# Kernel optimization log

Hardware: AMD Instinct MI355X
Metric: run time of the kernel (lower is better)

Reference implementation:

```python
import jax, jax.numpy as jnp
import numpy as np

N_HEADS = 16
EPS = 1e-5

def _ln(h, g, b):
    mu = jnp.mean(h, axis=-1, keepdims=True)
    var = jnp.var(h, axis=-1, keepdims=True)
    return (h - mu) * jax.lax.rsqrt(var + EPS) * g + b

def setup_inputs() -> dict:
    key = jax.random.key(0)
    ks = jax.random.split(key, 8)
    B, S, D, M = 2, 2048, 2048, 8192
    x = jax.random.normal(ks[0], (B, S, D), dtype=jnp.float32)
    # causal mask: True where attention is disallowed (j > i)
    mask = jnp.triu(jnp.ones((S, S), dtype=bool), k=1)[None, None]
    s = 1.0 / np.sqrt(D)
    Wq = jax.random.normal(ks[1], (D, D), dtype=jnp.float32) * s
    Wk = jax.random.normal(ks[2], (D, D), dtype=jnp.float32) * s
    Wv = jax.random.normal(ks[3], (D, D), dtype=jnp.float32) * s
    Wo = jax.random.normal(ks[4], (D, D), dtype=jnp.float32) * s
    W1 = jax.random.normal(ks[5], (D, M), dtype=jnp.float32) * s
    b1 = jnp.zeros((M,), dtype=jnp.float32)
    W2 = jax.random.normal(ks[6], (M, D), dtype=jnp.float32) * (1.0 / np.sqrt(M))
    b2 = jnp.zeros((D,), dtype=jnp.float32)
    ln1_g = jnp.ones((D,), jnp.float32); ln1_b = jnp.zeros((D,), jnp.float32)
    ln2_g = jnp.ones((D,), jnp.float32); ln2_b = jnp.zeros((D,), jnp.float32)
    return dict(x=x, self_attn_mask=mask, Wq=Wq, Wk=Wk, Wv=Wv, Wo=Wo,
                ln1_g=ln1_g, ln1_b=ln1_b, W1=W1, b1=b1, W2=W2, b2=b2,
                ln2_g=ln2_g, ln2_b=ln2_b)

def reference(x, self_attn_mask, Wq, Wk, Wv, Wo, ln1_g, ln1_b, W1, b1, W2, b2, ln2_g, ln2_b):
    B, S, D = x.shape
    n = N_HEADS
    d = D // n
    # --- self-attention with pre-norm residual ---
    h = _ln(x, ln1_g, ln1_b)
    # NOTE: source uses .view(b, n_heads, i, head_dim) with NO transpose -> plain reshape
    q = (h @ Wq).reshape(B, n, S, d)
    k = (h @ Wk).reshape(B, n, S, d)
    v = (h @ Wv).reshape(B, n, S, d)
    score = jnp.einsum('bnid,bnjd->bnij', q, k)
    # NOTE: source masks BEFORE scaling, so -1e9 is also divided by sqrt(d)
    score = jnp.where(self_attn_mask, jnp.float32(-1e9), score) / jnp.sqrt(jnp.float32(d))
    w = jax.nn.softmax(score, axis=3)
    o = jnp.einsum('bnij,bnjd->bnid', w, v)
    o = o.transpose(0, 2, 1, 3).reshape(B, S, D)  # b n i d -> b i (n d)
    x = x + o @ Wo
    # --- FFN with pre-norm residual ---
    h2 = _ln(x, ln2_g, ln2_b)
    ff = jnp.maximum(h2 @ W1 + b1, 0.0) @ W2 + b2
    return x + ff
```

## Files before the change

### kernel.cpp

```cpp
#include <hip/hip_runtime.h>
#include <cstdint>

using bf16x8 = __attribute__((ext_vector_type(8))) short;
using f32x4  = __attribute__((ext_vector_type(4))) float;

__device__ __forceinline__ unsigned short f2bf(float f) {
  union { float f; unsigned u; } v; v.f = f;
  unsigned u = v.u;
  u += 0x7fffu + ((u >> 16) & 1u);
  return (unsigned short)(u >> 16);
}

__device__ __forceinline__ void gload_lds16(const unsigned short* g, unsigned short* l) {
  __builtin_amdgcn_global_load_lds(
      (const __attribute__((address_space(1))) unsigned int*)g,
      (__attribute__((address_space(3))) unsigned int*)l, 16, 0, 0);
}

__global__ __launch_bounds__(256) void ln_kernel(
    const float* __restrict__ x, const float* __restrict__ g,
    const float* __restrict__ bb, unsigned short* __restrict__ h)
{
  const int D = 2048;
  const int row = blockIdx.x;
  const float* xr = x + (size_t)row * D;
  const int t = threadIdx.x;
  float4 v0 = ((const float4*)xr)[t];
  float4 v1 = ((const float4*)xr)[t + 256];
  float s  = v0.x+v0.y+v0.z+v0.w + v1.x+v1.y+v1.z+v1.w;
  float ss = v0.x*v0.x+v0.y*v0.y+v0.z*v0.z+v0.w*v0.w
           + v1.x*v1.x+v1.y*v1.y+v1.z*v1.z+v1.w*v1.w;
  #pragma unroll
  for (int off = 1; off < 64; off <<= 1) {
    s  += __shfl_xor(s, off);
    ss += __shfl_xor(ss, off);
  }
  __shared__ float red[8];
  const int wave = t >> 6, lane = t & 63;
  if (lane == 0) { red[wave] = s; red[4+wave] = ss; }
  __syncthreads();
  s  = red[0]+red[1]+red[2]+red[3];
  ss = red[4]+red[5]+red[6]+red[7];
  const float mu   = s * (1.f/2048.f);
  const float var  = ss * (1.f/2048.f) - mu*mu;
  const float rstd = rsqrtf(var + 1e-5f);
  unsigned short* hr = h + (size_t)row * D;
  #pragma unroll
  for (int q = 0; q < 2; ++q) {
    float4 v = q ? v1 : v0;
    int vecidx = t + q*256;
    float4 gg  = ((const float4*)g)[vecidx];
    float4 bv  = ((const float4*)bb)[vecidx];
    ushort4 o;
    o.x = f2bf((v.x-mu)*rstd*gg.x + bv.x);
    o.y = f2bf((v.y-mu)*rstd*gg.y + bv.y);
    o.z = f2bf((v.z-mu)*rstd*gg.z + bv.z);
    o.w = f2bf((v.w-mu)*rstd*gg.w + bv.w);
    *(ushort4*)(hr + vecidx*4) = o;
  }
}

__global__ __launch_bounds__(256) void transpose_cast(
    const float* __restrict__ W, unsigned short* __restrict__ WT,
    int K, int N)
{
  __shared__ float tile[32][33];
  const int tx = threadIdx.x, ty = threadIdx.y;
  const int n0 = blockIdx.x * 32, k0 = blockIdx.y * 32;
  #pragma unroll
  for (int r = 0; r < 4; ++r)
    tile[ty + r*8][tx] = W[(size_t)(k0 + ty + r*8) * N + n0 + tx];
  __syncthreads();
  #pragma unroll
  for (int r = 0; r < 4; ++r)
    WT[(size_t)(n0 + ty + r*8) * K + k0 + tx] = f2bf(tile[tx][ty + r*8]);
}

template<int BN, bool BIAS, bool RELU, bool RESID, bool OUTBF16>
__global__ __launch_bounds__(512, 2) void gemm8(
    const unsigned short* __restrict__ A, const unsigned short* __restrict__ BT,
    const float* __restrict__ bias, const float* __restrict__ resid,
    void* __restrict__ Cp, int M, int N, int K, int nbx)
{
  constexpr int BM = 256, BK = 64;
  constexpr int NREP = BN / 64;
  constexpr int BLD  = BN / 64;
  constexpr int LPK  = 4 + BLD;
  __shared__ __align__(16) unsigned short lds[2][(BM + BN) * BK];

  const int tid  = threadIdx.x;
  const int lane = tid & 63, wave = tid >> 6;
  const int l15 = lane & 15, lh = lane >> 4;
  const int wr = wave >> 2, wc = wave & 3;

  const int nwg = gridDim.x;
  const int q8  = nwg >> 3;
  const int wg  = blockIdx.x;
  const int swz = (wg & 7) * q8 + (wg >> 3);
  const size_t bm = (size_t)(swz / nbx) * BM;
  const size_t bn = (size_t)(swz % nbx) * BN;

  const int nk = K >> 6;

  auto stage = [&](int buf, int kt) {
    unsigned short* La = &lds[buf][0];
    unsigned short* Lb = &lds[buf][BM * BK];
    #pragma unroll
    for (int qq = 0; qq < 4; ++qq) {
      int idx = qq * 512 + tid;
      int row = idx >> 3, c = idx & 7;
      int gc = c ^ (row & 7);
      gload_lds16(A + (bm + row) * (size_t)K + (size_t)kt * BK + gc * 8,
                  La + idx * 8);
    }
    #pragma unroll
    for (int qq = 0; qq < BLD; ++qq) {
      int idx = qq * 512 + tid;
      int row = idx >> 3, c = idx & 7;
      int gc = c ^ (row & 7);
      gload_lds16(BT + (bn + row) * (size_t)K + (size_t)kt * BK + gc * 8,
                  Lb + idx * 8);
    }
  };

  f32x4 acc[8][NREP] = {};

  stage(0, 0);
  stage(1, 1);

  for (int kt = 0; kt < nk; ++kt) {
    const int buf = kt & 1;
    if (kt < nk - 1) {
      asm volatile("s_waitcnt vmcnt(%0)" :: "i"(LPK) : "memory");
    } else {
      asm volatile("s_waitcnt vmcnt(0)" ::: "memory");
    }
    __builtin_amdgcn_s_barrier();
    asm volatile("" ::: "memory");

    const unsigned short* La = &lds[buf][0];
    const unsigned short* Lb = &lds[buf][BM * BK];
    bf16x8 bfr[2][NREP];
    #pragma unroll
    for (int p = 0; p < 4; ++p) {
      if (p == 0) {
        #pragma unroll
        for (int kk = 0; kk < 2; ++kk)
          #pragma unroll
          for (int n = 0; n < NREP; ++n) {
            int brow = wc * (BN / 4) + n * 16 + l15;
            bfr[kk][n] = *(const bf16x8*)(Lb + brow * 64 +
                           ((kk * 32 + lh * 8) ^ ((brow & 7) << 3)));
          }
      }
      bf16x8 af[2][2];
      #pragma unroll
      for (int mi = 0; mi < 2; ++mi) {
        int arow = wr * 128 + (p * 2 + mi) * 16 + l15;
        #pragma unroll
        for (int kk = 0; kk < 2; ++kk)
          af[mi][kk] = *(const bf16x8*)(La + arow * 64 +
                         ((kk * 32 + lh * 8) ^ ((arow & 7) << 3)));
      }
      asm volatile("" ::: "memory");
      __builtin_amdgcn_s_barrier();
      __builtin_amdgcn_s_setprio(1);
      #pragma unroll
      for (int mi = 0; mi < 2; ++mi)
        #pragma unroll
        for (int n = 0; n < NREP; ++n)
          #pragma unroll
          for (int kk = 0; kk < 2; ++kk)
            acc[p*2+mi][n] = __builtin_amdgcn_mfma_f32_16x16x32_bf16(
                af[mi][kk], bfr[kk][n], acc[p*2+mi][n], 0, 0, 0);
      __builtin_amdgcn_s_setprio(0);
      asm volatile("" ::: "memory");
      __builtin_amdgcn_s_barrier();
    }
    if (kt + 2 < nk) stage(buf, kt + 2);
  }

  float bv[NREP];
  if (BIAS) {
    #pragma unroll
    for (int n = 0; n < NREP; ++n) bv[n] = bias[bn + wc*(BN/4) + n*16 + l15];
  }
  #pragma unroll
  for (int m = 0; m < 8; ++m) {
    #pragma unroll
    for (int r = 0; r < 4; ++r) {
      size_t rrow = bm + wr*128 + m*16 + lh*4 + r;
      #pragma unroll
      for (int n = 0; n < NREP; ++n) {
        size_t ccol = bn + wc*(BN/4) + n*16 + l15;
        float v = acc[m][n][r];
        if (BIAS)  v += bv[n];
        if (RELU)  v = fmaxf(v, 0.f);
        if (RESID) v += resid[rrow*(size_t)N + ccol];
        if (OUTBF16) ((unsigned short*)Cp)[rrow*(size_t)N + ccol] = f2bf(v);
        else         ((float*)Cp)[rrow*(size_t)N + ccol] = v;
      }
    }
  }
}

__global__ __launch_bounds__(256) void attn_kernel(
    const unsigned short* __restrict__ QKV, unsigned short* __restrict__ O)
{
  constexpr float SCALE = 0.08838834764831845f;
  __shared__ __align__(16) unsigned short Kl[64*128];
  __shared__ __align__(16) unsigned short Vf[64*128];
  __shared__ __align__(16) unsigned short Pl[4*1024];
  const int bid = blockIdx.x;
  const int qt = 31 - (bid >> 5);
  const int nh = bid & 15;
  const int b  = (bid >> 4) & 1;
  const int t = threadIdx.x;
  const int lane = t & 63, wave = t >> 6;
  const int l15 = lane & 15, lh = lane >> 4;
  const int i0 = qt*64 + wave*16;
  const size_t RS = 6144;
  const size_t base = (size_t)b * 2048 * RS;

  const unsigned short* qrow = QKV + base + (size_t)(nh*128 + (i0 >> 4)) * RS;
  bf16x8 qf[4];
  #pragma unroll
  for (int c = 0; c < 4; ++c)
    qf[c] = *(const bf16x8*)(qrow + l15*128 + c*32 + lh*8);

  f32x4 of[8] = {};
  float mrun[4], lrun[4];
  #pragma unroll
  for (int r = 0; r < 4; ++r) { mrun[r] = -INFINITY; lrun[r] = 0.f; }

  const int nkt = qt + 1;
  bf16x8 kr[4], vr[4];
  auto loadKV = [&](int kt) {
    #pragma unroll
    for (int q = 0; q < 4; ++q) {
      int c = t + q*256;
      int j = c >> 4, dd0 = (c & 15) * 8;
      const size_t grow = base + (size_t)(nh*128 + kt*4 + (j >> 4)) * RS + (j & 15)*128 + dd0;
      kr[q] = *(const bf16x8*)(QKV + grow + 2048);
      vr[q] = *(const bf16x8*)(QKV + grow + 4096);
    }
  };
  loadKV(0);

  for (int kt = 0; kt < nkt; ++kt) {
    __syncthreads();
    #pragma unroll
    for (int q = 0; q < 4; ++q) {
      int c = t + q*256;
      int j = c >> 4, dd0 = (c & 15) * 8;
      *(bf16x8*)((char*)Kl + ((j*256 + dd0*2) ^ ((j & 7) << 4))) = kr[q];
      int ks = j >> 5, jq = j & 31;
      int cc = dd0 >> 4;
      int wb = ks*8192 + cc*1024 + (((dd0 & 15) + 16*((jq >> 3) & 3)) & ~7)*16 + (jq & 7)*2;
      #pragma unroll
      for (int e = 0; e < 8; ++e)
        *(unsigned short*)((char*)Vf + wb + ((e ^ cc) * 16)) = (unsigned short)vr[q][e];
    }
    __syncthreads();
    if (kt + 1 < nkt) loadKV(kt + 1);

    f32x4 sc[4] = {};
    #pragma unroll
    for (int jt = 0; jt < 4; ++jt) {
      int row = jt*16 + l15;
      const char* kb = (const char*)Kl + row*256;
      const int sw = (row & 7) << 4;
      #pragma unroll
      for (int c = 0; c < 4; ++c) {
        bf16x8 kf = *(const bf16x8*)(kb + ((c*64 + lh*16) ^ sw));
        sc[jt] = __builtin_amdgcn_mfma_f32_16x16x32_bf16(qf[c], kf, sc[jt], 0, 0, 0);
      }
    }

    float fac[4];
    char* pw = (char*)Pl + wave*2048;
    #pragma unroll
    for (int r = 0; r < 4; ++r) {
      float s0 = sc[0][r]*SCALE, s1 = sc[1][r]*SCALE, s2 = sc[2][r]*SCALE, s3 = sc[3][r]*SCALE;
      if (kt == qt) {
        const int i = i0 + lh*4 + r;
        const int j = kt*64 + l15;
        s0 = (j      > i) ? -INFINITY : s0;
        s1 = (j + 16 > i) ? -INFINITY : s1;
        s2 = (j + 32 > i) ? -INFINITY : s2;
        s3 = (j + 48 > i) ? -INFINITY : s3;
      }
      float mx = fmaxf(fmaxf(s0, s1), fmaxf(s2, s3));
      #pragma unroll
      for (int mk = 1; mk < 16; mk <<= 1) mx = fmaxf(mx, __shfl_xor(mx, mk));
      const float mnew = fmaxf(mrun[r], mx);
      float p0 = __expf(s0 - mnew), p1 = __expf(s1 - mnew);
      float p2 = __expf(s2 - mnew), p3 = __expf(s3 - mnew);
      float psum = (p0 + p1) + (p2 + p3);
      #pragma unroll
      for (int mk = 1; mk < 16; mk <<= 1) psum += __shfl_xor(psum, mk);
      fac[r]  = __expf(mrun[r] - mnew);
      lrun[r] = lrun[r]*fac[r] + psum;
      mrun[r] = mnew;
      const int io = lh*4 + r;
      const int swp = (io & 7) << 4;
      char* pr = pw + io*128;
      *(unsigned short*)(pr + ((     l15*2) ^ swp)) = f2bf(p0);
      *(unsigned short*)(pr + ((32 + l15*2) ^ swp)) = f2bf(p1);
      *(unsigned short*)(pr + ((64 + l15*2) ^ swp)) = f2bf(p2);
      *(unsigned short*)(pr + ((96 + l15*2) ^ swp)) = f2bf(p3);
    }
    #pragma unroll
    for (int c = 0; c < 8; ++c)
      #pragma unroll
      for (int r = 0; r < 4; ++r)
        of[c][r] *= fac[r];

    const char* prd = pw + l15*128;
    const int psw = (l15 & 7) << 4;
    bf16x8 pa0 = *(const bf16x8*)(prd + ((     lh*16) ^ psw));
    bf16x8 pa1 = *(const bf16x8*)(prd + ((64 + lh*16) ^ psw));

    #pragma unroll
    for (int c = 0; c < 8; ++c) {
      const char* vb = (const char*)Vf + c*1024 + ((lane ^ c) * 16);
      bf16x8 v0 = *(const bf16x8*)(vb);
      bf16x8 v1 = *(const bf16x8*)(vb + 8192);
      of[c] = __builtin_amdgcn_mfma_f32_16x16x32_bf16(pa0, v0, of[c], 0, 0, 0);
      of[c] = __builtin_amdgcn_mfma_f32_16x16x32_bf16(pa1, v1, of[c], 0, 0, 0);
    }
  }

  unsigned short* orow = O + ((size_t)(b*2048 + i0))*2048 + nh*128;
  #pragma unroll
  for (int r = 0; r < 4; ++r) {
    const float inv = 1.f / lrun[r];
    #pragma unroll
    for (int c = 0; c < 8; ++c)
      orow[(size_t)(lh*4 + r)*2048 + c*16 + l15] = f2bf(of[c][r]*inv);
  }
}

extern "C" void kernel_launch(void* const* d_in, const int* in_sizes, int n_in,
                              void* d_out, int out_size, void* d_ws, size_t ws_size,
                              hipStream_t stream)
{
  const float* x    = (const float*)d_in[0];
  const float* Wq   = (const float*)d_in[2];
  const float* Wk   = (const float*)d_in[3];
  const float* Wv   = (const float*)d_in[4];
  const float* Wo   = (const float*)d_in[5];
  const float* ln1g = (const float*)d_in[6];
  const float* ln1b = (const float*)d_in[7];
  const float* W1   = (const float*)d_in[8];
  const float* b1   = (const float*)d_in[9];
  const float* W2   = (const float*)d_in[10];
  const float* b2   = (const float*)d_in[11];
  const float* ln2g = (const float*)d_in[12];
  const float* ln2b = (const float*)d_in[13];
  float* out = (float*)d_out;

  char* ws = (char*)d_ws;
  unsigned short* WqkvT  = (unsigned short*)(ws);
  unsigned short* WoT    = (unsigned short*)(ws + 25165824);
  unsigned short* W1T    = (unsigned short*)(ws + 33554432);
  unsigned short* W2T    = (unsigned short*)(ws + 67108864);
  unsigned short* h      = (unsigned short*)(ws + 100663296);
  float*          x2     = (float*)(ws + 117440512);
  unsigned short* QKV    = (unsigned short*)(ws + 150994944);
  unsigned short* attn_o = (unsigned short*)(ws + 201326592);
  unsigned short* ff1    = (unsigned short*)(ws + 150994944);

  dim3 tb(32, 8);
  transpose_cast<<<dim3(64, 64),  tb, 0, stream>>>(Wq, WqkvT,                2048, 2048);
  transpose_cast<<<dim3(64, 64),  tb, 0, stream>>>(Wk, WqkvT + 2048*2048,    2048, 2048);
  transpose_cast<<<dim3(64, 64),  tb, 0, stream>>>(Wv, WqkvT + 2*2048*2048,  2048, 2048);
  transpose_cast<<<dim3(64, 64),  tb, 0, stream>>>(Wo, WoT,                  2048, 2048);
  transpose_cast<<<dim3(256, 64), tb, 0, stream>>>(W1, W1T,                  2048, 8192);
  transpose_cast<<<dim3(64, 256), tb, 0, stream>>>(W2, W2T,                  8192, 2048);

  ln_kernel<<<4096, 256, 0, stream>>>(x, ln1g, ln1b, h);
  gemm8<256,false,false,false,true><<<384, 512, 0, stream>>>(
      h, WqkvT, nullptr, nullptr, QKV, 4096, 6144, 2048, 24);
  attn_kernel<<<1024, 256, 0, stream>>>(QKV, attn_o);
  gemm8<128,false,false,true,false><<<256, 512, 0, stream>>>(
      attn_o, WoT, nullptr, x, x2, 4096, 2048, 2048, 16);
  ln_kernel<<<4096, 256, 0, stream>>>(x2, ln2g, ln2b, h);
  gemm8<256,true,true,false,true><<<512, 512, 0, stream>>>(
      h, W1T, b1, nullptr, ff1, 4096, 8192, 2048, 32);
  gemm8<128,true,false,true,false><<<256, 512, 0, stream>>>(
      ff1, W2T, b2, x2, out, 4096, 2048, 8192, 16);
}
```

Baseline: 647.9 us.

## Interleave next-tile global loads with MFMA phases and switch GEMM tiles to BN=256

The GEMM template now fixes BN at 256 and parametrises BM, so the N=2048 GEMMs use 128x256 tiles instead of 256x128. The prefetch of the tile two steps ahead is split into pieces and issued between the per-phase MFMA blocks instead of all at once after the compute loop. The intent is to overlap global-to-LDS traffic with matrix math and to change the A/B reuse balance for the narrow output GEMMs. In exchange, the LDS buffer being refilled is still read by other waves within the same iteration, which depends on the barriers inside each phase for correctness.

```diff
diff --git a/kernel.cpp b/kernel.cpp
--- a/kernel.cpp
+++ b/kernel.cpp
@@ -76,16 +76,16 @@
     WT[(size_t)(n0 + ty + r*8) * K + k0 + tx] = f2bf(tile[tx][ty + r*8]);
 }
 
-template<int BN, bool BIAS, bool RELU, bool RESID, bool OUTBF16>
+template<int BM, bool BIAS, bool RELU, bool RESID, bool OUTBF16>
 __global__ __launch_bounds__(512, 2) void gemm8(
     const unsigned short* __restrict__ A, const unsigned short* __restrict__ BT,
     const float* __restrict__ bias, const float* __restrict__ resid,
     void* __restrict__ Cp, int M, int N, int K, int nbx)
 {
-  constexpr int BM = 256, BK = 64;
-  constexpr int NREP = BN / 64;
-  constexpr int BLD  = BN / 64;
-  constexpr int LPK  = 4 + BLD;
+  constexpr int BN = 256, BK = 64;
+  constexpr int MPH = BM / 64;
+  constexpr int AQ  = BM / 64;
+  constexpr int LPK = AQ + 4;
   __shared__ __align__(16) unsigned short lds[2][(BM + BN) * BK];
 
   const int tid  = threadIdx.x;
@@ -99,56 +99,57 @@
   const int swz = (wg & 7) * q8 + (wg >> 3);
   const size_t bm = (size_t)(swz / nbx) * BM;
   const size_t bn = (size_t)(swz % nbx) * BN;
-
   const int nk = K >> 6;
 
-  auto stage = [&](int buf, int kt) {
-    unsigned short* La = &lds[buf][0];
-    unsigned short* Lb = &lds[buf][BM * BK];
-    #pragma unroll
-    for (int qq = 0; qq < 4; ++qq) {
-      int idx = qq * 512 + tid;
-      int row = idx >> 3, c = idx & 7;
-      int gc = c ^ (row & 7);
-      gload_lds16(A + (bm + row) * (size_t)K + (size_t)kt * BK + gc * 8,
-                  La + idx * 8);
-    }
-    #pragma unroll
-    for (int qq = 0; qq < BLD; ++qq) {
-      int idx = qq * 512 + tid;
-      int row = idx >> 3, c = idx & 7;
-      int gc = c ^ (row & 7);
-      gload_lds16(BT + (bn + row) * (size_t)K + (size_t)kt * BK + gc * 8,
-                  Lb + idx * 8);
-    }
+  auto stageA = [&](int buf, int kt, int qq) {
+    int idx = qq * 512 + tid;
+    int row = idx >> 3, c = idx & 7, gc = c ^ (row & 7);
+    gload_lds16(A + (bm + row) * (size_t)K + (size_t)kt * BK + gc * 8,
+                &lds[buf][0] + idx * 8);
   };
-
-  f32x4 acc[8][NREP] = {};
-
-  stage(0, 0);
-  stage(1, 1);
+  auto stageB = [&](int buf, int kt, int qq) {
+    int idx = qq * 512 + tid;
+    int row = idx >> 3, c = idx & 7, gc = c ^ (row & 7);
+    gload_lds16(BT + (bn + row) * (size_t)K + (size_t)kt * BK + gc * 8,
+                &lds[buf][BM * BK] + idx * 8);
+  };
+
+  f32x4 acc[MPH * 2][4] = {};
+
+  #pragma unroll
+  for (int qq = 0; qq < AQ; ++qq) stageA(0, 0, qq);
+  #pragma unroll
+  for (int qq = 0; qq < 4; ++qq)  stageB(0, 0, qq);
+  #pragma unroll
+  for (int qq = 0; qq < AQ; ++qq) stageA(1, 1, qq);
+  #pragma unroll
+  for (int qq = 0; qq < 4; ++qq)  stageB(1, 1, qq);
 
   for (int kt = 0; kt < nk; ++kt) {
     const int buf = kt & 1;
-    if (kt < nk - 1) {
-      asm volatile("s_waitcnt vmcnt(%0)" :: "i"(LPK) : "memory");
-    } else {
-      asm volatile("s_waitcnt vmcnt(0)" ::: "memory");
-    }
+    if (kt < nk - 1) asm volatile("s_waitcnt vmcnt(%0)" :: "i"(LPK) : "memory");
+    else             asm volatile("s_waitcnt vmcnt(0)" ::: "memory");
     __builtin_amdgcn_s_barrier();
     asm volatile("" ::: "memory");
 
     const unsigned short* La = &lds[buf][0];
     const unsigned short* Lb = &lds[buf][BM * BK];
-    bf16x8 bfr[2][NREP];
-    #pragma unroll
-    for (int p = 0; p < 4; ++p) {
+    bf16x8 bfr[2][4];
+    const bool pf = (kt + 2 < nk);
+
+    #pragma unroll
+    for (int p = 0; p < MPH; ++p) {
+      if (p > 0 && pf) {
+        if (MPH == 4) { stageA(buf, kt + 2, p - 1); stageB(buf, kt + 2, p - 1); }
+        else          { stageA(buf, kt + 2, 0);
+                        stageB(buf, kt + 2, 0); stageB(buf, kt + 2, 1); }
+      }
       if (p == 0) {
         #pragma unroll
         for (int kk = 0; kk < 2; ++kk)
           #pragma unroll
-          for (int n = 0; n < NREP; ++n) {
-            int brow = wc * (BN / 4) + n * 16 + l15;
+          for (int n = 0; n < 4; ++n) {
+            int brow = wc * 64 + n * 16 + l15;
             bfr[kk][n] = *(const bf16x8*)(Lb + brow * 64 +
                            ((kk * 32 + lh * 8) ^ ((brow & 7) << 3)));
           }
@@ -156,7 +157,7 @@
       bf16x8 af[2][2];
       #pragma unroll
       for (int mi = 0; mi < 2; ++mi) {
-        int arow = wr * 128 + (p * 2 + mi) * 16 + l15;
+        int arow = (p * 4 + wr * 2 + mi) * 16 + l15;
         #pragma unroll
         for (int kk = 0; kk < 2; ++kk)
           af[mi][kk] = *(const bf16x8*)(La + arow * 64 +
@@ -168,7 +169,7 @@
       #pragma unroll
       for (int mi = 0; mi < 2; ++mi)
         #pragma unroll
-        for (int n = 0; n < NREP; ++n)
+        for (int n = 0; n < 4; ++n)
           #pragma unroll
           for (int kk = 0; kk < 2; ++kk)
             acc[p*2+mi][n] = __builtin_amdgcn_mfma_f32_16x16x32_bf16(
@@ -177,28 +178,35 @@
       asm volatile("" ::: "memory");
       __builtin_amdgcn_s_barrier();
     }
-    if (kt + 2 < nk) stage(buf, kt + 2);
-  }
-
-  float bv[NREP];
+    if (pf) {
+      if (MPH == 4) { stageA(buf, kt + 2, 3); stageB(buf, kt + 2, 3); }
+      else          { stageA(buf, kt + 2, 1);
+                      stageB(buf, kt + 2, 2); stageB(buf, kt + 2, 3); }
+    }
+  }
+
+  float bv[4];
   if (BIAS) {
     #pragma unroll
-    for (int n = 0; n < NREP; ++n) bv[n] = bias[bn + wc*(BN/4) + n*16 + l15];
-  }
-  #pragma unroll
-  for (int m = 0; m < 8; ++m) {
-    #pragma unroll
-    for (int r = 0; r < 4; ++r) {
-      size_t rrow = bm + wr*128 + m*16 + lh*4 + r;
-      #pragma unroll
-      for (int n = 0; n < NREP; ++n) {
-        size_t ccol = bn + wc*(BN/4) + n*16 + l15;
-        float v = acc[m][n][r];
-        if (BIAS)  v += bv[n];
-        if (RELU)  v = fmaxf(v, 0.f);
-        if (RESID) v += resid[rrow*(size_t)N + ccol];
-        if (OUTBF16) ((unsigned short*)Cp)[rrow*(size_t)N + ccol] = f2bf(v);
-        else         ((float*)Cp)[rrow*(size_t)N + ccol] = v;
+    for (int n = 0; n < 4; ++n) bv[n] = bias[bn + wc*64 + n*16 + l15];
+  }
+  #pragma unroll
+  for (int p = 0; p < MPH; ++p) {
+    #pragma unroll
+    for (int mi = 0; mi < 2; ++mi) {
+      #pragma unroll
+      for (int r = 0; r < 4; ++r) {
+        size_t rrow = bm + (size_t)(p*4 + wr*2 + mi)*16 + lh*4 + r;
+        #pragma unroll
+        for (int n = 0; n < 4; ++n) {
+          size_t ccol = bn + wc*64 + n*16 + l15;
+          float v = acc[p*2+mi][n][r];
+          if (BIAS)  v += bv[n];
+          if (RELU)  v = fmaxf(v, 0.f);
+          if (RESID) v += resid[rrow*(size_t)N + ccol];
+          if (OUTBF16) ((unsigned short*)Cp)[rrow*(size_t)N + ccol] = f2bf(v);
+          else         ((float*)Cp)[rrow*(size_t)N + ccol] = v;
+        }
       }
     }
   }
@@ -384,10 +392,10 @@
       h, WqkvT, nullptr, nullptr, QKV, 4096, 6144, 2048, 24);
   attn_kernel<<<1024, 256, 0, stream>>>(QKV, attn_o);
   gemm8<128,false,false,true,false><<<256, 512, 0, stream>>>(
-      attn_o, WoT, nullptr, x, x2, 4096, 2048, 2048, 16);
+      attn_o, WoT, nullptr, x, x2, 4096, 2048, 2048, 8);
   ln_kernel<<<4096, 256, 0, stream>>>(x2, ln2g, ln2b, h);
   gemm8<256,true,true,false,true><<<512, 512, 0, stream>>>(
       h, W1T, b1, nullptr, ff1, 4096, 8192, 2048, 32);
   gemm8<128,true,false,true,false><<<256, 512, 0, stream>>>(
-      ff1, W2T, b2, x2, out, 4096, 2048, 8192, 16);
-}
+      ff1, W2T, b2, x2, out, 4096, 2048, 8192, 8);
+}
```

Result: faster. 626.5 us (-3.3%).
